# Kernel tuning notes

Hardware: AMD Instinct MI355X
Metric: run time of the kernel (lower is better)

Reference implementation:

```python
import jax, jax.numpy as jnp
import numpy as np

N = 100_000
E = 1_600_000
F_IN = 128
HEADS = 8
OUT_H = 8   # per-head channels, concat -> 64
N_CLS = 40
K_HOPS = 10  # truncation order of heat-kernel Taylor series
NEG_SLOPE = 0.2
T_INIT = 5.0


def setup_inputs() -> dict:
    key = jax.random.key(0)
    ks = jax.random.split(key, 10)
    x = jax.random.normal(ks[0], (N, F_IN), jnp.float32)
    edge_index = jax.random.randint(ks[1], (2, E), 0, N, jnp.int32)
    t = jnp.full((F_IN,), T_INIT, jnp.float32)  # per-channel learnable diffusion time
    W1 = jax.random.normal(ks[2], (F_IN, HEADS * OUT_H), jnp.float32) / np.sqrt(F_IN).astype(np.float32)
    a_src1 = jax.random.normal(ks[3], (HEADS, OUT_H), jnp.float32) * 0.1
    a_dst1 = jax.random.normal(ks[4], (HEADS, OUT_H), jnp.float32) * 0.1
    b1 = jnp.zeros((HEADS * OUT_H,), jnp.float32)
    W2 = jax.random.normal(ks[5], (HEADS * OUT_H, N_CLS), jnp.float32) / np.sqrt(HEADS * OUT_H).astype(np.float32)
    a_src2 = jax.random.normal(ks[6], (1, N_CLS), jnp.float32) * 0.1
    a_dst2 = jax.random.normal(ks[7], (1, N_CLS), jnp.float32) * 0.1
    b2 = jnp.zeros((N_CLS,), jnp.float32)
    return {"x": x, "edge_index": edge_index, "t": t, "W1": W1, "a_src1": a_src1,
            "a_dst1": a_dst1, "b1": b1, "W2": W2, "a_src2": a_src2, "a_dst2": a_dst2, "b2": b2}


def _add_self_loops(edge_index, n):
    loop = jnp.arange(n, dtype=edge_index.dtype)
    return jnp.concatenate([edge_index, jnp.stack([loop, loop])], axis=1)


def _diffusion(x, src, dst, t, n):
    # heat kernel: exp(-t) * sum_k t^k/k! * A_hat^k x, per-channel t
    deg = jax.ops.segment_sum(jnp.ones_like(src, jnp.float32), dst, num_segments=n)
    dinv = jnp.where(deg > 0, jax.lax.rsqrt(jnp.maximum(deg, 1.0)), 0.0)
    norm = dinv[src] * dinv[dst]  # [E+N]

    def prop(h):
        return jax.ops.segment_sum(norm[:, None] * h[src], dst, num_segments=n)

    coef0 = jnp.exp(-t)  # [F]

    def step(carry, k):
        h, coef, acc = carry
        h = prop(h)
        coef = coef * t / k
        return (h, coef, acc + coef * h), None

    (_, _, out), _ = jax.lax.scan(step, (x, coef0, coef0 * x),
                                  jnp.arange(1, K_HOPS + 1, dtype=jnp.float32))
    return out


def _gat_layer(x, src, dst, W, a_s, a_d, b, heads, out_ch, concat, n):
    h = (x @ W).reshape(n, heads, out_ch)                  # [N,H,C]
    al_s = jnp.einsum('nhc,hc->nh', h, a_s)                # src attn logits
    al_d = jnp.einsum('nhc,hc->nh', h, a_d)
    e = jax.nn.leaky_relu(al_s[src] + al_d[dst], NEG_SLOPE)  # [E+N, H]
    emax = jax.ops.segment_max(e, dst, num_segments=n)       # stable softmax per target node
    ex = jnp.exp(e - emax[dst])
    denom = jax.ops.segment_sum(ex, dst, num_segments=n)
    alpha = ex / jnp.maximum(denom[dst], 1e-16)               # [E+N, H]
    out = jax.ops.segment_sum(alpha[:, :, None] * h[src], dst, num_segments=n)  # [N,H,C]
    out = out.reshape(n, heads * out_ch) if concat else out.mean(axis=1)
    return out + b


def reference(x, edge_index, t, W1, a_src1, a_dst1, b1, W2, a_src2, a_dst2, b2):
    n = x.shape[0]
    ei = _add_self_loops(edge_index, n)
    src, dst = ei[0], ei[1]
    h = _diffusion(x, src, dst, t, n)
    h = _gat_layer(h, src, dst, W1, a_src1, a_dst1, b1, HEADS, OUT_H, True, n)
    h = jax.nn.elu(h)
    h = _gat_layer(h, src, dst, W2, a_src2, a_dst2, b2, 1, N_CLS, False, n)
    return jax.nn.log_softmax(h, axis=1)
```

## Files before the change

kernel.cpp:

```cpp
#include <hip/hip_runtime.h>
#include <hip/hip_bf16.h>


static __device__ __forceinline__ unsigned pack_bf16x2(float a, float b) {
    __hip_bfloat162 p(__float2bfloat16(a), __float2bfloat16(b));
    return *reinterpret_cast<unsigned*>(&p);
}

__global__ void init_node_kernel(int* deg, int* cursor, int n) {
    int i = blockIdx.x * 256 + threadIdx.x;
    if (i < n) { deg[i] = 1; cursor[i] = 0; }
}

__global__ void edge_deg_kernel(const int* __restrict__ dst, int* deg, int E) {
    int e = blockIdx.x * 256 + threadIdx.x;
    if (e < E) atomicAdd(&deg[dst[e]], 1);
}

__global__ void alloc_kernel(const int* __restrict__ deg, float* dinv,
                             int* row_off, int* gcount, int n) {
    int i = blockIdx.x * 256 + threadIdx.x;
    if (i >= n) return;
    int dg = deg[i];
    dinv[i] = rsqrtf((float)dg);
    row_off[i] = atomicAdd(gcount, dg);
}

__global__ void scatter_kernel(const int* __restrict__ ei, const int* __restrict__ row_off,
                               int* cursor, const float* __restrict__ dinv,
                               int2* csr_pair, int E, int n) {
    int e = blockIdx.x * 256 + threadIdx.x;
    if (e >= E + n) return;
    int s, d;
    if (e < E) { s = ei[e]; d = ei[E + e]; } else { s = e - E; d = s; }
    int pos = atomicAdd(&cursor[d], 1);
    int slot = row_off[d] + pos;
    csr_pair[slot] = make_int2(s, __float_as_int(dinv[s] * dinv[d]));
}

__global__ void coef_kernel(const float* __restrict__ t, float* coefs) {
    int c = threadIdx.x;
    float tc = t[c];
    float v = expf(-tc);
    coefs[c] = v;
    for (int k = 1; k <= 10; ++k) { v *= tc / (float)k; coefs[k * 128 + c] = v; }
}

__global__ void init_diff_kernel(const float4* __restrict__ x4, const float* __restrict__ coefs,
                                 uint2* __restrict__ h, float4* __restrict__ acc4, int total4) {
    int i = blockIdx.x * 256 + threadIdx.x;
    if (i >= total4) return;
    float4 xv = x4[i];
    h[i] = make_uint2(pack_bf16x2(xv.x, xv.y), pack_bf16x2(xv.z, xv.w));
    const float4 c = *(const float4*)&coefs[(i & 31) * 4];
    acc4[i] = make_float4(c.x * xv.x, c.y * xv.y, c.z * xv.z, c.w * xv.w);
}

__global__ void hop_kernel(const int* __restrict__ row_off, const int* __restrict__ deg,
                           const int2* __restrict__ csr_pair,
                           const unsigned* __restrict__ h, unsigned* __restrict__ h_next,
                           float2* __restrict__ acc2, const float2* __restrict__ coefk2,
                           int n, int write_h) {
    int wid = (blockIdx.x << 2) + (threadIdx.x >> 6);
    int lane = threadIdx.x & 63;
    if (wid >= n) return;
    int off = row_off[wid];
    int cnt = deg[wid];
    float2 a0 = {0.f, 0.f}, a1 = {0.f, 0.f}, a2 = {0.f, 0.f}, a3 = {0.f, 0.f};
    for (int base = 0; base < cnt; base += 64) {
        int nb = min(64, cnt - base);
        int2 p = {0, 0};
        if (lane < nb) p = csr_pair[off + base + lane];
        int tt = 0;
        for (; tt + 7 < nb; tt += 8) {
            int s0 = __builtin_amdgcn_readlane(p.x, tt);
            int s1 = __builtin_amdgcn_readlane(p.x, tt + 1);
            int s2 = __builtin_amdgcn_readlane(p.x, tt + 2);
            int s3 = __builtin_amdgcn_readlane(p.x, tt + 3);
            int s4 = __builtin_amdgcn_readlane(p.x, tt + 4);
            int s5 = __builtin_amdgcn_readlane(p.x, tt + 5);
            int s6 = __builtin_amdgcn_readlane(p.x, tt + 6);
            int s7 = __builtin_amdgcn_readlane(p.x, tt + 7);
            float w0 = __int_as_float(__builtin_amdgcn_readlane(p.y, tt));
            float w1 = __int_as_float(__builtin_amdgcn_readlane(p.y, tt + 1));
            float w2 = __int_as_float(__builtin_amdgcn_readlane(p.y, tt + 2));
            float w3 = __int_as_float(__builtin_amdgcn_readlane(p.y, tt + 3));
            float w4 = __int_as_float(__builtin_amdgcn_readlane(p.y, tt + 4));
            float w5 = __int_as_float(__builtin_amdgcn_readlane(p.y, tt + 5));
            float w6 = __int_as_float(__builtin_amdgcn_readlane(p.y, tt + 6));
            float w7 = __int_as_float(__builtin_amdgcn_readlane(p.y, tt + 7));
            unsigned u0 = h[(size_t)s0 * 64 + lane];
            unsigned u1 = h[(size_t)s1 * 64 + lane];
            unsigned u2 = h[(size_t)s2 * 64 + lane];
            unsigned u3 = h[(size_t)s3 * 64 + lane];
            unsigned u4 = h[(size_t)s4 * 64 + lane];
            unsigned u5 = h[(size_t)s5 * 64 + lane];
            unsigned u6 = h[(size_t)s6 * 64 + lane];
            unsigned u7 = h[(size_t)s7 * 64 + lane];
            a0.x = fmaf(w0, __uint_as_float(u0 << 16), a0.x);
            a0.y = fmaf(w0, __uint_as_float(u0 & 0xffff0000u), a0.y);
            a1.x = fmaf(w1, __uint_as_float(u1 << 16), a1.x);
            a1.y = fmaf(w1, __uint_as_float(u1 & 0xffff0000u), a1.y);
            a2.x = fmaf(w2, __uint_as_float(u2 << 16), a2.x);
            a2.y = fmaf(w2, __uint_as_float(u2 & 0xffff0000u), a2.y);
            a3.x = fmaf(w3, __uint_as_float(u3 << 16), a3.x);
            a3.y = fmaf(w3, __uint_as_float(u3 & 0xffff0000u), a3.y);
            a0.x = fmaf(w4, __uint_as_float(u4 << 16), a0.x);
            a0.y = fmaf(w4, __uint_as_float(u4 & 0xffff0000u), a0.y);
            a1.x = fmaf(w5, __uint_as_float(u5 << 16), a1.x);
            a1.y = fmaf(w5, __uint_as_float(u5 & 0xffff0000u), a1.y);
            a2.x = fmaf(w6, __uint_as_float(u6 << 16), a2.x);
            a2.y = fmaf(w6, __uint_as_float(u6 & 0xffff0000u), a2.y);
            a3.x = fmaf(w7, __uint_as_float(u7 << 16), a3.x);
            a3.y = fmaf(w7, __uint_as_float(u7 & 0xffff0000u), a3.y);
        }
        for (; tt < nb; ++tt) {
            int s = __builtin_amdgcn_readlane(p.x, tt);
            float w = __int_as_float(__builtin_amdgcn_readlane(p.y, tt));
            unsigned u = h[(size_t)s * 64 + lane];
            a0.x = fmaf(w, __uint_as_float(u << 16), a0.x);
            a0.y = fmaf(w, __uint_as_float(u & 0xffff0000u), a0.y);
        }
    }
    float2 s;
    s.x = (a0.x + a1.x) + (a2.x + a3.x);
    s.y = (a0.y + a1.y) + (a2.y + a3.y);
    size_t o = (size_t)wid * 64 + lane;
    if (write_h) h_next[o] = pack_bf16x2(s.x, s.y);
    float2 c = coefk2[lane];
    float2 av = acc2[o];
    av.x = fmaf(c.x, s.x, av.x);
    av.y = fmaf(c.y, s.y, av.y);
    acc2[o] = av;
}

__global__ __launch_bounds__(256) void gemm1_kernel(
    const float* __restrict__ acc, const float* __restrict__ W1,
    const float* __restrict__ a_s, const float* __restrict__ a_d,
    unsigned* __restrict__ h1b, float* __restrict__ als, float* __restrict__ ald, int n) {
    __shared__ float Wl[128 * 64];
    __shared__ float Al[4][16 * 128];
    for (int i = threadIdx.x; i < 128 * 64; i += 256) Wl[i] = W1[i];
    int w = threadIdx.x >> 6;
    int lane = threadIdx.x & 63;
    int node0 = (blockIdx.x * 4 + w) * 16;
    const float4* accv4 = (const float4*)acc;
    float4* Av4 = (float4*)Al[w];
#pragma unroll
    for (int i = 0; i < 8; ++i) {
        int f4 = i * 64 + lane;
        int g4 = node0 * 32 + f4;
        float4 v = (g4 < n * 32) ? accv4[g4] : make_float4(0.f, 0.f, 0.f, 0.f);
        Av4[f4] = v;
    }
    __syncthreads();
    float sums[16];
#pragma unroll
    for (int nd = 0; nd < 16; ++nd) sums[nd] = 0.f;
#pragma unroll 1
    for (int kc = 0; kc < 16; ++kc) {
        float wr[8];
#pragma unroll
        for (int i = 0; i < 8; ++i) wr[i] = Wl[(kc * 8 + i) * 64 + lane];
#pragma unroll
        for (int nd = 0; nd < 16; ++nd) {
            float4 a = *(const float4*)&Al[w][nd * 128 + kc * 8];
            float4 b = *(const float4*)&Al[w][nd * 128 + kc * 8 + 4];
            float s = sums[nd];
            s = fmaf(wr[0], a.x, s); s = fmaf(wr[1], a.y, s);
            s = fmaf(wr[2], a.z, s); s = fmaf(wr[3], a.w, s);
            s = fmaf(wr[4], b.x, s); s = fmaf(wr[5], b.y, s);
            s = fmaf(wr[6], b.z, s); s = fmaf(wr[7], b.w, s);
            sums[nd] = s;
        }
    }
    float asv = a_s[lane], adv = a_d[lane];
#pragma unroll
    for (int nd = 0; nd < 16; ++nd) {
        int node = node0 + nd;
        if (node >= n) break;
        float sum = sums[nd];
        float partner = __shfl_xor(sum, 1);
        if ((lane & 1) == 0) h1b[(size_t)node * 32 + (lane >> 1)] = pack_bf16x2(sum, partner);
        float vs = sum * asv;
        float vd = sum * adv;
        vs += __shfl_xor(vs, 1); vs += __shfl_xor(vs, 2); vs += __shfl_xor(vs, 4);
        vd += __shfl_xor(vd, 1); vd += __shfl_xor(vd, 2); vd += __shfl_xor(vd, 4);
        if ((lane & 7) == 0) {
            als[(size_t)node * 8 + (lane >> 3)] = vs;
            ald[(size_t)node * 8 + (lane >> 3)] = vd;
        }
    }
}

__global__ void agg1_kernel(const int* __restrict__ row_off, const int* __restrict__ deg,
                            const int2* __restrict__ csr_pair,
                            const unsigned* __restrict__ h1b, const float* __restrict__ als,
                            const float* __restrict__ ald, const float* __restrict__ b1,
                            float2* __restrict__ helu2, int n) {
    int wid = (blockIdx.x << 2) + (threadIdx.x >> 6);
    int lane = threadIdx.x & 63;
    if (wid >= n) return;
    int half = lane >> 5;
    int l = lane & 31;
    int head = l >> 2;
    int off = row_off[wid];
    int cnt = deg[wid];
    float aldv = ald[(size_t)wid * 8 + head];
    float dA = 0.f, dB = 0.f;
    float2 aA = {0.f, 0.f}, aB = {0.f, 0.f};
    for (int base = 0; base < cnt; base += 64) {
        int nb = min(64, cnt - base);
        int srcv = 0;
        if (lane < nb) srcv = csr_pair[off + base + lane].x;
        int j = 0;
        for (; j + 3 < nb; j += 4) {
            int sA0 = __builtin_amdgcn_readlane(srcv, j);
            int sA1 = __builtin_amdgcn_readlane(srcv, j + 1);
            int sB0 = __builtin_amdgcn_readlane(srcv, j + 2);
            int sB1 = __builtin_amdgcn_readlane(srcv, j + 3);
            int sA = half ? sA1 : sA0;
            int sB = half ? sB1 : sB0;
            float eA = als[(size_t)sA * 8 + head] + aldv;
            float eB = als[(size_t)sB * 8 + head] + aldv;
            eA = eA > 0.f ? eA : 0.2f * eA;
            eB = eB > 0.f ? eB : 0.2f * eB;
            float pA = __expf(eA);
            float pB = __expf(eB);
            unsigned uA = h1b[(size_t)sA * 32 + l];
            unsigned uB = h1b[(size_t)sB * 32 + l];
            dA += pA; dB += pB;
            aA.x = fmaf(pA, __uint_as_float(uA << 16), aA.x);
            aA.y = fmaf(pA, __uint_as_float(uA & 0xffff0000u), aA.y);
            aB.x = fmaf(pB, __uint_as_float(uB << 16), aB.x);
            aB.y = fmaf(pB, __uint_as_float(uB & 0xffff0000u), aB.y);
        }
        for (; j < nb; j += 2) {
            int s0 = __builtin_amdgcn_readlane(srcv, j);
            int s1 = (j + 1 < nb) ? __builtin_amdgcn_readlane(srcv, j + 1) : -1;
            int s = half ? s1 : s0;
            bool valid = s >= 0;
            int ss = valid ? s : 0;
            float e = als[(size_t)ss * 8 + head] + aldv;
            e = e > 0.f ? e : 0.2f * e;
            float p = valid ? __expf(e) : 0.f;
            unsigned u = h1b[(size_t)ss * 32 + l];
            dA += p;
            aA.x = fmaf(p, __uint_as_float(u << 16), aA.x);
            aA.y = fmaf(p, __uint_as_float(u & 0xffff0000u), aA.y);
        }
    }
    float d = dA + dB;
    float2 accv = make_float2(aA.x + aB.x, aA.y + aB.y);
    d += __shfl_xor(d, 32);
    accv.x += __shfl_xor(accv.x, 32);
    accv.y += __shfl_xor(accv.y, 32);
    if (half == 0) {
        float inv = 1.f / d;
        float ox = fmaf(accv.x, inv, b1[2 * l]);
        float oy = fmaf(accv.y, inv, b1[2 * l + 1]);
        ox = ox > 0.f ? ox : expm1f(ox);
        oy = oy > 0.f ? oy : expm1f(oy);
        helu2[(size_t)wid * 32 + l] = make_float2(ox, oy);
    }
}

__global__ __launch_bounds__(256) void gemm2_kernel(
    const float* __restrict__ helu, const float* __restrict__ W2,
    const float* __restrict__ a_s, const float* __restrict__ a_d,
    unsigned* __restrict__ h2b, float* __restrict__ als, float* __restrict__ ald, int n) {
    __shared__ float Wl[64 * 40];
    __shared__ float Al[4][16 * 64];
    for (int i = threadIdx.x; i < 64 * 40; i += 256) Wl[i] = W2[i];
    int w = threadIdx.x >> 6;
    int lane = threadIdx.x & 63;
    int node0 = (blockIdx.x * 4 + w) * 16;
    const float4* hv4 = (const float4*)helu;
    float4* Av4 = (float4*)Al[w];
#pragma unroll
    for (int i = 0; i < 4; ++i) {
        int f4 = i * 64 + lane;
        int g4 = node0 * 16 + f4;
        float4 v = (g4 < n * 16) ? hv4[g4] : make_float4(0.f, 0.f, 0.f, 0.f);
        Av4[f4] = v;
    }
    __syncthreads();
    bool act = lane < 40;
    int li = act ? lane : 0;
    float sums[16];
#pragma unroll
    for (int nd = 0; nd < 16; ++nd) sums[nd] = 0.f;
#pragma unroll 1
    for (int kc = 0; kc < 8; ++kc) {
        float wr[8];
#pragma unroll
        for (int i = 0; i < 8; ++i) wr[i] = Wl[(kc * 8 + i) * 40 + li];
#pragma unroll
        for (int nd = 0; nd < 16; ++nd) {
            float4 a = *(const float4*)&Al[w][nd * 64 + kc * 8];
            float4 b = *(const float4*)&Al[w][nd * 64 + kc * 8 + 4];
            float s = sums[nd];
            s = fmaf(wr[0], a.x, s); s = fmaf(wr[1], a.y, s);
            s = fmaf(wr[2], a.z, s); s = fmaf(wr[3], a.w, s);
            s = fmaf(wr[4], b.x, s); s = fmaf(wr[5], b.y, s);
            s = fmaf(wr[6], b.z, s); s = fmaf(wr[7], b.w, s);
            sums[nd] = s;
        }
    }
    float asv = act ? a_s[lane] : 0.f;
    float adv = act ? a_d[lane] : 0.f;
#pragma unroll
    for (int nd = 0; nd < 16; ++nd) {
        int node = node0 + nd;
        if (node >= n) break;
        float sum = sums[nd];
        float partner = __shfl_xor(sum, 1);
        if (act && (lane & 1) == 0) h2b[(size_t)node * 20 + (lane >> 1)] = pack_bf16x2(sum, partner);
        float vs = act ? sum * asv : 0.f;
        float vd = act ? sum * adv : 0.f;
#pragma unroll
        for (int i = 32; i >= 1; i >>= 1) { vs += __shfl_xor(vs, i); vd += __shfl_xor(vd, i); }
        if (lane == 0) { als[node] = vs; ald[node] = vd; }
    }
}

__global__ void agg2_kernel(const int* __restrict__ row_off, const int* __restrict__ deg,
                            const int2* __restrict__ csr_pair,
                            const unsigned* __restrict__ h2b, const float* __restrict__ als,
                            const float* __restrict__ ald, const float* __restrict__ b2,
                            float* __restrict__ out, int n) {
    int wid = (blockIdx.x << 2) + (threadIdx.x >> 6);
    int lane = threadIdx.x & 63;
    if (wid >= n) return;
    int half = lane >> 5;
    int l = lane & 31;
    bool act = l < 20;
    int li = act ? l : 0;
    int off = row_off[wid];
    int cnt = deg[wid];
    float aldv = ald[wid];
    float dA = 0.f, dB = 0.f;
    float2 aA = {0.f, 0.f}, aB = {0.f, 0.f};
    for (int base = 0; base < cnt; base += 64) {
        int nb = min(64, cnt - base);
        int srcv = 0;
        if (lane < nb) srcv = csr_pair[off + base + lane].x;
        int j = 0;
        for (; j + 3 < nb; j += 4) {
            int sA0 = __builtin_amdgcn_readlane(srcv, j);
            int sA1 = __builtin_amdgcn_readlane(srcv, j + 1);
            int sB0 = __builtin_amdgcn_readlane(srcv, j + 2);
            int sB1 = __builtin_amdgcn_readlane(srcv, j + 3);
            int sA = half ? sA1 : sA0;
            int sB = half ? sB1 : sB0;
            float eA = als[sA] + aldv;
            float eB = als[sB] + aldv;
            eA = eA > 0.f ? eA : 0.2f * eA;
            eB = eB > 0.f ? eB : 0.2f * eB;
            float pA = __expf(eA);
            float pB = __expf(eB);
            unsigned uA = h2b[(size_t)sA * 20 + li];
            unsigned uB = h2b[(size_t)sB * 20 + li];
            dA += pA; dB += pB;
            aA.x = fmaf(pA, __uint_as_float(uA << 16), aA.x);
            aA.y = fmaf(pA, __uint_as_float(uA & 0xffff0000u), aA.y);
            aB.x = fmaf(pB, __uint_as_float(uB << 16), aB.x);
            aB.y = fmaf(pB, __uint_as_float(uB & 0xffff0000u), aB.y);
        }
        for (; j < nb; j += 2) {
            int s0 = __builtin_amdgcn_readlane(srcv, j);
            int s1 = (j + 1 < nb) ? __builtin_amdgcn_readlane(srcv, j + 1) : -1;
            int s = half ? s1 : s0;
            bool valid = s >= 0;
            int ss = valid ? s : 0;
            float e = als[ss] + aldv;
            e = e > 0.f ? e : 0.2f * e;
            float p = valid ? __expf(e) : 0.f;
            unsigned u = h2b[(size_t)ss * 20 + li];
            dA += p;
            aA.x = fmaf(p, __uint_as_float(u << 16), aA.x);
            aA.y = fmaf(p, __uint_as_float(u & 0xffff0000u), aA.y);
        }
    }
    float d = dA + dB;
    float2 accv = make_float2(aA.x + aB.x, aA.y + aB.y);
    d += __shfl_xor(d, 32);
    accv.x += __shfl_xor(accv.x, 32);
    accv.y += __shfl_xor(accv.y, 32);
    float inv = 1.f / d;
    bool live = (half == 0) && act;
    float ox = live ? fmaf(accv.x, inv, b2[2 * l]) : -1e30f;
    float oy = live ? fmaf(accv.y, inv, b2[2 * l + 1]) : -1e30f;
    float vv = fmaxf(ox, oy);
#pragma unroll
    for (int i = 16; i >= 1; i >>= 1) vv = fmaxf(vv, __shfl_xor(vv, i));
    float ex = live ? (__expf(ox - vv) + __expf(oy - vv)) : 0.f;
#pragma unroll
    for (int i = 16; i >= 1; i >>= 1) ex += __shfl_xor(ex, i);
    if (live) {
        float lse = vv + logf(ex);
        *(float2*)&out[(size_t)wid * 40 + 2 * l] = make_float2(ox - lse, oy - lse);
    }
}

extern "C" void kernel_launch(void* const* d_in, const int* in_sizes, int n_in,
                              void* d_out, int out_size, void* d_ws, size_t ws_size,
                              hipStream_t stream) {
    const float* x    = (const float*)d_in[0];
    const int*   ei   = (const int*)d_in[1];
    const float* t    = (const float*)d_in[2];
    const float* W1   = (const float*)d_in[3];
    const float* a_s1 = (const float*)d_in[4];
    const float* a_d1 = (const float*)d_in[5];
    const float* b1   = (const float*)d_in[6];
    const float* W2   = (const float*)d_in[7];
    const float* a_s2 = (const float*)d_in[8];
    const float* a_d2 = (const float*)d_in[9];
    const float* b2   = (const float*)d_in[10];
    float* out = (float*)d_out;

    const int N = in_sizes[0] / 128;
    const int E = in_sizes[1] / 2;

    char* w = (char*)d_ws;
    auto carve = [&](size_t bytes) {
        void* p = (void*)w;
        w += (bytes + 255) & ~(size_t)255;
        return p;
    };
    int*      deg      = (int*)carve((size_t)N * 4);
    int*      cursor   = (int*)carve((size_t)N * 4);
    int*      row_off  = (int*)carve((size_t)N * 4);
    int*      gcount   = (int*)carve(256);
    float*    dinv     = (float*)carve((size_t)N * 4);
    int2*     csr_pair = (int2*)carve((size_t)(E + N) * 8);
    float*    coefs    = (float*)carve(11 * 128 * 4);
    float*    als1     = (float*)carve((size_t)N * 8 * 4);
    float*    ald1     = (float*)carve((size_t)N * 8 * 4);
    float*    als2     = (float*)carve((size_t)N * 4);
    float*    ald2     = (float*)carve((size_t)N * 4);
    unsigned* hA       = (unsigned*)carve((size_t)N * 64 * 4);
    unsigned* hB       = (unsigned*)carve((size_t)N * 64 * 4);
    float*    acc      = (float*)carve((size_t)N * 128 * 4);
    unsigned* h1b      = (unsigned*)carve((size_t)N * 32 * 4);
    float*    helu     = (float*)carve((size_t)N * 64 * 4);
    unsigned* h2b      = (unsigned*)carve((size_t)N * 20 * 4);

    dim3 blk(256);
    int gN = (N + 255) / 256;
    int gE = (E + 255) / 256;
    int gEN = (E + N + 255) / 256;
    int gW = (N + 3) / 4;
    int gT = (N + 63) / 64;

    init_node_kernel<<<gN, blk, 0, stream>>>(deg, cursor, N);
    hipMemsetAsync(gcount, 0, 4, stream);
    edge_deg_kernel<<<gE, blk, 0, stream>>>(ei + E, deg, E);
    alloc_kernel<<<gN, blk, 0, stream>>>(deg, dinv, row_off, gcount, N);
    scatter_kernel<<<gEN, blk, 0, stream>>>(ei, row_off, cursor, dinv, csr_pair, E, N);
    coef_kernel<<<1, 128, 0, stream>>>(t, coefs);
    init_diff_kernel<<<(N * 32 + 255) / 256, blk, 0, stream>>>(
        (const float4*)x, coefs, (uint2*)hA, (float4*)acc, N * 32);

    unsigned* hc = hA;
    unsigned* hn = hB;
    for (int k = 1; k <= 10; ++k) {
        hop_kernel<<<gW, blk, 0, stream>>>(row_off, deg, csr_pair, hc, hn, (float2*)acc,
                                           (const float2*)(coefs + k * 128), N,
                                           k < 10 ? 1 : 0);
        unsigned* tmp = hc; hc = hn; hn = tmp;
    }

    gemm1_kernel<<<gT, blk, 0, stream>>>(acc, W1, a_s1, a_d1, h1b, als1, ald1, N);
    agg1_kernel<<<gW, blk, 0, stream>>>(row_off, deg, csr_pair, h1b, als1, ald1, b1,
                                        (float2*)helu, N);
    gemm2_kernel<<<gT, blk, 0, stream>>>(helu, W2, a_s2, a_d2, h2b, als2, ald2, N);
    agg2_kernel<<<gW, blk, 0, stream>>>(row_off, deg, csr_pair, h2b, als2, ald2, b2, out, N);
}
```

Before: 1.311 ms.

## Fuse diffusion hops into one persistent cooperative kernel with register accumulators

Replaces the init kernel and ten per-hop launches with a single persistent cooperative kernel of 1536 blocks. Each wave owns up to 17 nodes and keeps their acc values in registers across hops, using grid.sync between hops, which removes the per-hop acc read-modify-write and the launch gaps. CSR construction also records each edge's slot from the degree atomic, so the separate cursor atomics in scatter go away. The cost is a hard node limit (NMAX*NWAVE must cover N), more register pressure with launch_bounds(256,6), grid-sync overhead, and a gather loop unrolled 4 instead of 8.

```diff
diff --git a/kernel.cpp b/kernel.cpp
--- a/kernel.cpp
+++ b/kernel.cpp
@@ -1,20 +1,27 @@
 #include <hip/hip_runtime.h>
 #include <hip/hip_bf16.h>
-
+#include <hip/hip_cooperative_groups.h>
+
+namespace cg = cooperative_groups;
+
+
+#define NBLK  1536
+#define NWAVE (NBLK * 4)
+#define NMAX  17
 
 static __device__ __forceinline__ unsigned pack_bf16x2(float a, float b) {
     __hip_bfloat162 p(__float2bfloat16(a), __float2bfloat16(b));
     return *reinterpret_cast<unsigned*>(&p);
 }
 
-__global__ void init_node_kernel(int* deg, int* cursor, int n) {
+__global__ void init_node_kernel(int* deg, int n) {
     int i = blockIdx.x * 256 + threadIdx.x;
-    if (i < n) { deg[i] = 1; cursor[i] = 0; }
-}
-
-__global__ void edge_deg_kernel(const int* __restrict__ dst, int* deg, int E) {
+    if (i < n) deg[i] = 1;
+}
+
+__global__ void edge_deg_kernel(const int* __restrict__ dst, int* deg, int* epos, int E) {
     int e = blockIdx.x * 256 + threadIdx.x;
-    if (e < E) atomicAdd(&deg[dst[e]], 1);
+    if (e < E) epos[e] = atomicAdd(&deg[dst[e]], 1);
 }
 
 __global__ void alloc_kernel(const int* __restrict__ deg, float* dinv,
@@ -27,15 +34,17 @@
 }
 
 __global__ void scatter_kernel(const int* __restrict__ ei, const int* __restrict__ row_off,
-                               int* cursor, const float* __restrict__ dinv,
-                               int2* csr_pair, int E, int n) {
+                               const int* __restrict__ epos, const float* __restrict__ dinv,
+                               int2* __restrict__ csr_pair, int E, int n) {
     int e = blockIdx.x * 256 + threadIdx.x;
-    if (e >= E + n) return;
-    int s, d;
-    if (e < E) { s = ei[e]; d = ei[E + e]; } else { s = e - E; d = s; }
-    int pos = atomicAdd(&cursor[d], 1);
-    int slot = row_off[d] + pos;
-    csr_pair[slot] = make_int2(s, __float_as_int(dinv[s] * dinv[d]));
+    if (e < E) {
+        int s = ei[e], d = ei[E + e];
+        csr_pair[row_off[d] + epos[e]] = make_int2(s, __float_as_int(dinv[s] * dinv[d]));
+    } else if (e < E + n) {
+        int i = e - E;
+        float di = dinv[i];
+        csr_pair[row_off[i]] = make_int2(i, __float_as_int(di * di));
+    }
 }
 
 __global__ void coef_kernel(const float* __restrict__ t, float* coefs) {
@@ -46,92 +55,96 @@
     for (int k = 1; k <= 10; ++k) { v *= tc / (float)k; coefs[k * 128 + c] = v; }
 }
 
-__global__ void init_diff_kernel(const float4* __restrict__ x4, const float* __restrict__ coefs,
-                                 uint2* __restrict__ h, float4* __restrict__ acc4, int total4) {
-    int i = blockIdx.x * 256 + threadIdx.x;
-    if (i >= total4) return;
-    float4 xv = x4[i];
-    h[i] = make_uint2(pack_bf16x2(xv.x, xv.y), pack_bf16x2(xv.z, xv.w));
-    const float4 c = *(const float4*)&coefs[(i & 31) * 4];
-    acc4[i] = make_float4(c.x * xv.x, c.y * xv.y, c.z * xv.z, c.w * xv.w);
-}
-
-__global__ void hop_kernel(const int* __restrict__ row_off, const int* __restrict__ deg,
-                           const int2* __restrict__ csr_pair,
-                           const unsigned* __restrict__ h, unsigned* __restrict__ h_next,
-                           float2* __restrict__ acc2, const float2* __restrict__ coefk2,
-                           int n, int write_h) {
+__global__ __launch_bounds__(256, 6) void diffuse_kernel(
+    const int* __restrict__ row_off, const int* __restrict__ deg,
+    const int2* __restrict__ csr_pair, const float2* __restrict__ x2,
+    const float* __restrict__ coefs, unsigned* __restrict__ hA,
+    unsigned* __restrict__ hB, float2* __restrict__ accg, int n) {
+    cg::grid_group grid = cg::this_grid();
     int wid = (blockIdx.x << 2) + (threadIdx.x >> 6);
     int lane = threadIdx.x & 63;
-    if (wid >= n) return;
-    int off = row_off[wid];
-    int cnt = deg[wid];
-    float2 a0 = {0.f, 0.f}, a1 = {0.f, 0.f}, a2 = {0.f, 0.f}, a3 = {0.f, 0.f};
-    for (int base = 0; base < cnt; base += 64) {
-        int nb = min(64, cnt - base);
-        int2 p = {0, 0};
-        if (lane < nb) p = csr_pair[off + base + lane];
-        int tt = 0;
-        for (; tt + 7 < nb; tt += 8) {
-            int s0 = __builtin_amdgcn_readlane(p.x, tt);
-            int s1 = __builtin_amdgcn_readlane(p.x, tt + 1);
-            int s2 = __builtin_amdgcn_readlane(p.x, tt + 2);
-            int s3 = __builtin_amdgcn_readlane(p.x, tt + 3);
-            int s4 = __builtin_amdgcn_readlane(p.x, tt + 4);
-            int s5 = __builtin_amdgcn_readlane(p.x, tt + 5);
-            int s6 = __builtin_amdgcn_readlane(p.x, tt + 6);
-            int s7 = __builtin_amdgcn_readlane(p.x, tt + 7);
-            float w0 = __int_as_float(__builtin_amdgcn_readlane(p.y, tt));
-            float w1 = __int_as_float(__builtin_amdgcn_readlane(p.y, tt + 1));
-            float w2 = __int_as_float(__builtin_amdgcn_readlane(p.y, tt + 2));
-            float w3 = __int_as_float(__builtin_amdgcn_readlane(p.y, tt + 3));
-            float w4 = __int_as_float(__builtin_amdgcn_readlane(p.y, tt + 4));
-            float w5 = __int_as_float(__builtin_amdgcn_readlane(p.y, tt + 5));
-            float w6 = __int_as_float(__builtin_amdgcn_readlane(p.y, tt + 6));
-            float w7 = __int_as_float(__builtin_amdgcn_readlane(p.y, tt + 7));
-            unsigned u0 = h[(size_t)s0 * 64 + lane];
-            unsigned u1 = h[(size_t)s1 * 64 + lane];
-            unsigned u2 = h[(size_t)s2 * 64 + lane];
-            unsigned u3 = h[(size_t)s3 * 64 + lane];
-            unsigned u4 = h[(size_t)s4 * 64 + lane];
-            unsigned u5 = h[(size_t)s5 * 64 + lane];
-            unsigned u6 = h[(size_t)s6 * 64 + lane];
-            unsigned u7 = h[(size_t)s7 * 64 + lane];
-            a0.x = fmaf(w0, __uint_as_float(u0 << 16), a0.x);
-            a0.y = fmaf(w0, __uint_as_float(u0 & 0xffff0000u), a0.y);
-            a1.x = fmaf(w1, __uint_as_float(u1 << 16), a1.x);
-            a1.y = fmaf(w1, __uint_as_float(u1 & 0xffff0000u), a1.y);
-            a2.x = fmaf(w2, __uint_as_float(u2 << 16), a2.x);
-            a2.y = fmaf(w2, __uint_as_float(u2 & 0xffff0000u), a2.y);
-            a3.x = fmaf(w3, __uint_as_float(u3 << 16), a3.x);
-            a3.y = fmaf(w3, __uint_as_float(u3 & 0xffff0000u), a3.y);
-            a0.x = fmaf(w4, __uint_as_float(u4 << 16), a0.x);
-            a0.y = fmaf(w4, __uint_as_float(u4 & 0xffff0000u), a0.y);
-            a1.x = fmaf(w5, __uint_as_float(u5 << 16), a1.x);
-            a1.y = fmaf(w5, __uint_as_float(u5 & 0xffff0000u), a1.y);
-            a2.x = fmaf(w6, __uint_as_float(u6 << 16), a2.x);
-            a2.y = fmaf(w6, __uint_as_float(u6 & 0xffff0000u), a2.y);
-            a3.x = fmaf(w7, __uint_as_float(u7 << 16), a3.x);
-            a3.y = fmaf(w7, __uint_as_float(u7 & 0xffff0000u), a3.y);
-        }
-        for (; tt < nb; ++tt) {
-            int s = __builtin_amdgcn_readlane(p.x, tt);
-            float w = __int_as_float(__builtin_amdgcn_readlane(p.y, tt));
-            unsigned u = h[(size_t)s * 64 + lane];
-            a0.x = fmaf(w, __uint_as_float(u << 16), a0.x);
-            a0.y = fmaf(w, __uint_as_float(u & 0xffff0000u), a0.y);
-        }
-    }
-    float2 s;
-    s.x = (a0.x + a1.x) + (a2.x + a3.x);
-    s.y = (a0.y + a1.y) + (a2.y + a3.y);
-    size_t o = (size_t)wid * 64 + lane;
-    if (write_h) h_next[o] = pack_bf16x2(s.x, s.y);
-    float2 c = coefk2[lane];
-    float2 av = acc2[o];
-    av.x = fmaf(c.x, s.x, av.x);
-    av.y = fmaf(c.y, s.y, av.y);
-    acc2[o] = av;
+    const float2* coefs2 = (const float2*)coefs;
+
+    float2 acc[NMAX];
+    float2 c0 = coefs2[lane];
+#pragma unroll
+    for (int j = 0; j < NMAX; ++j) {
+        int node = wid + j * NWAVE;
+        if (node < n) {
+            float2 xv = x2[(size_t)node * 64 + lane];
+            acc[j] = make_float2(c0.x * xv.x, c0.y * xv.y);
+            hA[(size_t)node * 64 + lane] = pack_bf16x2(xv.x, xv.y);
+        } else {
+            acc[j] = make_float2(0.f, 0.f);
+        }
+    }
+    grid.sync();
+
+    const unsigned* cur = hA;
+    unsigned* nxt = hB;
+#pragma unroll 1
+    for (int k = 1; k <= 10; ++k) {
+        float2 ck = coefs2[(size_t)k * 64 + lane];
+        bool wh = (k < 10);
+#pragma unroll
+        for (int j = 0; j < NMAX; ++j) {
+            int node = wid + j * NWAVE;
+            if (node < n) {
+                int off = row_off[node];
+                int cnt = deg[node];
+                float2 a0 = {0.f, 0.f}, a1 = {0.f, 0.f};
+                float2 a2 = {0.f, 0.f}, a3 = {0.f, 0.f};
+                for (int base = 0; base < cnt; base += 64) {
+                    int nb = min(64, cnt - base);
+                    int2 p = {0, 0};
+                    if (lane < nb) p = csr_pair[off + base + lane];
+                    int tt = 0;
+                    for (; tt + 3 < nb; tt += 4) {
+                        int s0 = __builtin_amdgcn_readlane(p.x, tt);
+                        int s1 = __builtin_amdgcn_readlane(p.x, tt + 1);
+                        int s2 = __builtin_amdgcn_readlane(p.x, tt + 2);
+                        int s3 = __builtin_amdgcn_readlane(p.x, tt + 3);
+                        float w0 = __int_as_float(__builtin_amdgcn_readlane(p.y, tt));
+                        float w1 = __int_as_float(__builtin_amdgcn_readlane(p.y, tt + 1));
+                        float w2 = __int_as_float(__builtin_amdgcn_readlane(p.y, tt + 2));
+                        float w3 = __int_as_float(__builtin_amdgcn_readlane(p.y, tt + 3));
+                        unsigned u0 = cur[(size_t)s0 * 64 + lane];
+                        unsigned u1 = cur[(size_t)s1 * 64 + lane];
+                        unsigned u2 = cur[(size_t)s2 * 64 + lane];
+                        unsigned u3 = cur[(size_t)s3 * 64 + lane];
+                        a0.x = fmaf(w0, __uint_as_float(u0 << 16), a0.x);
+                        a0.y = fmaf(w0, __uint_as_float(u0 & 0xffff0000u), a0.y);
+                        a1.x = fmaf(w1, __uint_as_float(u1 << 16), a1.x);
+                        a1.y = fmaf(w1, __uint_as_float(u1 & 0xffff0000u), a1.y);
+                        a2.x = fmaf(w2, __uint_as_float(u2 << 16), a2.x);
+                        a2.y = fmaf(w2, __uint_as_float(u2 & 0xffff0000u), a2.y);
+                        a3.x = fmaf(w3, __uint_as_float(u3 << 16), a3.x);
+                        a3.y = fmaf(w3, __uint_as_float(u3 & 0xffff0000u), a3.y);
+                    }
+                    for (; tt < nb; ++tt) {
+                        int s = __builtin_amdgcn_readlane(p.x, tt);
+                        float w = __int_as_float(__builtin_amdgcn_readlane(p.y, tt));
+                        unsigned u = cur[(size_t)s * 64 + lane];
+                        a0.x = fmaf(w, __uint_as_float(u << 16), a0.x);
+                        a0.y = fmaf(w, __uint_as_float(u & 0xffff0000u), a0.y);
+                    }
+                }
+                float2 s;
+                s.x = (a0.x + a1.x) + (a2.x + a3.x);
+                s.y = (a0.y + a1.y) + (a2.y + a3.y);
+                if (wh) nxt[(size_t)node * 64 + lane] = pack_bf16x2(s.x, s.y);
+                acc[j].x = fmaf(ck.x, s.x, acc[j].x);
+                acc[j].y = fmaf(ck.y, s.y, acc[j].y);
+            }
+        }
+        if (k < 10) grid.sync();
+        const unsigned* t = cur; cur = nxt; nxt = (unsigned*)t;
+    }
+#pragma unroll
+    for (int j = 0; j < NMAX; ++j) {
+        int node = wid + j * NWAVE;
+        if (node < n) accg[(size_t)node * 64 + lane] = acc[j];
+    }
 }
 
 __global__ __launch_bounds__(256) void gemm1_kernel(
@@ -429,10 +442,10 @@
         return p;
     };
     int*      deg      = (int*)carve((size_t)N * 4);
-    int*      cursor   = (int*)carve((size_t)N * 4);
     int*      row_off  = (int*)carve((size_t)N * 4);
     int*      gcount   = (int*)carve(256);
     float*    dinv     = (float*)carve((size_t)N * 4);
+    int*      epos     = (int*)carve((size_t)E * 4);
     int2*     csr_pair = (int2*)carve((size_t)(E + N) * 8);
     float*    coefs    = (float*)carve(11 * 128 * 4);
     float*    als1     = (float*)carve((size_t)N * 8 * 4);
@@ -453,22 +466,28 @@
     int gW = (N + 3) / 4;
     int gT = (N + 63) / 64;
 
-    init_node_kernel<<<gN, blk, 0, stream>>>(deg, cursor, N);
+    init_node_kernel<<<gN, blk, 0, stream>>>(deg, N);
     hipMemsetAsync(gcount, 0, 4, stream);
-    edge_deg_kernel<<<gE, blk, 0, stream>>>(ei + E, deg, E);
+    edge_deg_kernel<<<gE, blk, 0, stream>>>(ei + E, deg, epos, E);
     alloc_kernel<<<gN, blk, 0, stream>>>(deg, dinv, row_off, gcount, N);
-    scatter_kernel<<<gEN, blk, 0, stream>>>(ei, row_off, cursor, dinv, csr_pair, E, N);
+    scatter_kernel<<<gEN, blk, 0, stream>>>(ei, row_off, epos, dinv, csr_pair, E, N);
     coef_kernel<<<1, 128, 0, stream>>>(t, coefs);
-    init_diff_kernel<<<(N * 32 + 255) / 256, blk, 0, stream>>>(
-        (const float4*)x, coefs, (uint2*)hA, (float4*)acc, N * 32);
-
-    unsigned* hc = hA;
-    unsigned* hn = hB;
-    for (int k = 1; k <= 10; ++k) {
-        hop_kernel<<<gW, blk, 0, stream>>>(row_off, deg, csr_pair, hc, hn, (float2*)acc,
-                                           (const float2*)(coefs + k * 128), N,
-                                           k < 10 ? 1 : 0);
-        unsigned* tmp = hc; hc = hn; hn = tmp;
+
+    {
+        const float2* x2v = (const float2*)x;
+        float2* acc2v = (float2*)acc;
+        int Nv = N;
+        const int* row_off_v = row_off;
+        const int* deg_v = deg;
+        const int2* csr_v = csr_pair;
+        const float* coefs_v = coefs;
+        unsigned* hA_v = hA;
+        unsigned* hB_v = hB;
+        void* kargs[] = {(void*)&row_off_v, (void*)&deg_v, (void*)&csr_v, (void*)&x2v,
+                         (void*)&coefs_v, (void*)&hA_v, (void*)&hB_v, (void*)&acc2v,
+                         (void*)&Nv};
+        hipLaunchCooperativeKernel((const void*)diffuse_kernel, dim3(NBLK), dim3(256),
+                                   kargs, 0, stream);
     }
 
     gemm1_kernel<<<gT, blk, 0, stream>>>(acc, W1, a_s1, a_d1, h1b, als1, ald1, N);
```

Measured after the change: 3.305 ms. +152.1%, slower.

## Store all diffusion hops in bf16 and combine once; drop CSR cursor atomics

Applied to the files above, without the earlier changes.

When the workspace is large enough, each diffusion hop writes its bf16 output into its own buffer. A single combine kernel then forms the Taylor-weighted sum from x and all ten hops, so the fp32 accumulator is no longer read and written on every hop. CSR construction also reuses the slot index returned by the degree atomic, which removes the second atomic pass over a cursor array. In exchange the change needs roughly eleven bf16 feature buffers of workspace and an extra epos array. If the workspace is too small, it falls back to the old per-hop accumulation.

```diff
diff --git a/kernel.cpp b/kernel.cpp
--- a/kernel.cpp
+++ b/kernel.cpp
@@ -7,14 +7,14 @@
     return *reinterpret_cast<unsigned*>(&p);
 }
 
-__global__ void init_node_kernel(int* deg, int* cursor, int n) {
+__global__ void init_node_kernel(int* deg, int n) {
     int i = blockIdx.x * 256 + threadIdx.x;
-    if (i < n) { deg[i] = 1; cursor[i] = 0; }
-}
-
-__global__ void edge_deg_kernel(const int* __restrict__ dst, int* deg, int E) {
+    if (i < n) deg[i] = 1;
+}
+
+__global__ void edge_deg_kernel(const int* __restrict__ dst, int* deg, int* epos, int E) {
     int e = blockIdx.x * 256 + threadIdx.x;
-    if (e < E) atomicAdd(&deg[dst[e]], 1);
+    if (e < E) epos[e] = atomicAdd(&deg[dst[e]], 1);
 }
 
 __global__ void alloc_kernel(const int* __restrict__ deg, float* dinv,
@@ -27,15 +27,17 @@
 }
 
 __global__ void scatter_kernel(const int* __restrict__ ei, const int* __restrict__ row_off,
-                               int* cursor, const float* __restrict__ dinv,
-                               int2* csr_pair, int E, int n) {
+                               const int* __restrict__ epos, const float* __restrict__ dinv,
+                               int2* __restrict__ csr_pair, int E, int n) {
     int e = blockIdx.x * 256 + threadIdx.x;
-    if (e >= E + n) return;
-    int s, d;
-    if (e < E) { s = ei[e]; d = ei[E + e]; } else { s = e - E; d = s; }
-    int pos = atomicAdd(&cursor[d], 1);
-    int slot = row_off[d] + pos;
-    csr_pair[slot] = make_int2(s, __float_as_int(dinv[s] * dinv[d]));
+    if (e < E) {
+        int s = ei[e], d = ei[E + e];
+        csr_pair[row_off[d] + epos[e]] = make_int2(s, __float_as_int(dinv[s] * dinv[d]));
+    } else if (e < E + n) {
+        int i = e - E;
+        float di = dinv[i];
+        csr_pair[row_off[i]] = make_int2(i, __float_as_int(di * di));
+    }
 }
 
 __global__ void coef_kernel(const float* __restrict__ t, float* coefs) {
@@ -46,24 +48,28 @@
     for (int k = 1; k <= 10; ++k) { v *= tc / (float)k; coefs[k * 128 + c] = v; }
 }
 
-__global__ void init_diff_kernel(const float4* __restrict__ x4, const float* __restrict__ coefs,
-                                 uint2* __restrict__ h, float4* __restrict__ acc4, int total4) {
+__global__ void init_diff_a_kernel(const float4* __restrict__ x4, uint2* __restrict__ h0,
+                                   int total4) {
     int i = blockIdx.x * 256 + threadIdx.x;
     if (i >= total4) return;
     float4 xv = x4[i];
-    h[i] = make_uint2(pack_bf16x2(xv.x, xv.y), pack_bf16x2(xv.z, xv.w));
+    h0[i] = make_uint2(pack_bf16x2(xv.x, xv.y), pack_bf16x2(xv.z, xv.w));
+}
+
+__global__ void init_diff_b_kernel(const float4* __restrict__ x4, const float* __restrict__ coefs,
+                                   uint2* __restrict__ h0, float4* __restrict__ acc4, int total4) {
+    int i = blockIdx.x * 256 + threadIdx.x;
+    if (i >= total4) return;
+    float4 xv = x4[i];
+    h0[i] = make_uint2(pack_bf16x2(xv.x, xv.y), pack_bf16x2(xv.z, xv.w));
     const float4 c = *(const float4*)&coefs[(i & 31) * 4];
     acc4[i] = make_float4(c.x * xv.x, c.y * xv.y, c.z * xv.z, c.w * xv.w);
 }
 
-__global__ void hop_kernel(const int* __restrict__ row_off, const int* __restrict__ deg,
-                           const int2* __restrict__ csr_pair,
-                           const unsigned* __restrict__ h, unsigned* __restrict__ h_next,
-                           float2* __restrict__ acc2, const float2* __restrict__ coefk2,
-                           int n, int write_h) {
-    int wid = (blockIdx.x << 2) + (threadIdx.x >> 6);
-    int lane = threadIdx.x & 63;
-    if (wid >= n) return;
+static __device__ __forceinline__ float2 gather_row(
+    const int* __restrict__ row_off, const int* __restrict__ deg,
+    const int2* __restrict__ csr_pair, const unsigned* __restrict__ h,
+    int wid, int lane) {
     int off = row_off[wid];
     int cnt = deg[wid];
     float2 a0 = {0.f, 0.f}, a1 = {0.f, 0.f}, a2 = {0.f, 0.f}, a3 = {0.f, 0.f};
@@ -125,13 +131,56 @@
     float2 s;
     s.x = (a0.x + a1.x) + (a2.x + a3.x);
     s.y = (a0.y + a1.y) + (a2.y + a3.y);
+    return s;
+}
+
+__global__ void hop_a_kernel(const int* __restrict__ row_off, const int* __restrict__ deg,
+                             const int2* __restrict__ csr_pair,
+                             const unsigned* __restrict__ h_prev, unsigned* __restrict__ h_out,
+                             int n) {
+    int wid = (blockIdx.x << 2) + (threadIdx.x >> 6);
+    int lane = threadIdx.x & 63;
+    if (wid >= n) return;
+    float2 s = gather_row(row_off, deg, csr_pair, h_prev, wid, lane);
+    h_out[(size_t)wid * 64 + lane] = pack_bf16x2(s.x, s.y);
+}
+
+__global__ void hop_b_kernel(const int* __restrict__ row_off, const int* __restrict__ deg,
+                             const int2* __restrict__ csr_pair,
+                             const unsigned* __restrict__ h_prev, unsigned* __restrict__ h_out,
+                             float2* __restrict__ acc2, const float2* __restrict__ coefk2,
+                             int n, int write_h) {
+    int wid = (blockIdx.x << 2) + (threadIdx.x >> 6);
+    int lane = threadIdx.x & 63;
+    if (wid >= n) return;
+    float2 s = gather_row(row_off, deg, csr_pair, h_prev, wid, lane);
     size_t o = (size_t)wid * 64 + lane;
-    if (write_h) h_next[o] = pack_bf16x2(s.x, s.y);
+    if (write_h) h_out[o] = pack_bf16x2(s.x, s.y);
     float2 c = coefk2[lane];
     float2 av = acc2[o];
     av.x = fmaf(c.x, s.x, av.x);
     av.y = fmaf(c.y, s.y, av.y);
     acc2[o] = av;
+}
+
+__global__ void combine_kernel(const float2* __restrict__ x2, const float* __restrict__ coefs,
+                               const unsigned* __restrict__ hseq, size_t stride,
+                               float2* __restrict__ acc2, int total) {
+    int i = blockIdx.x * 256 + threadIdx.x;
+    if (i >= total) return;
+    int c2 = i & 63;
+    const float2* coefs2 = (const float2*)coefs;
+    float2 c0 = coefs2[c2];
+    float2 xv = x2[i];
+    float2 a = make_float2(c0.x * xv.x, c0.y * xv.y);
+#pragma unroll
+    for (int k = 1; k <= 10; ++k) {
+        float2 ck = coefs2[(size_t)k * 64 + c2];
+        unsigned u = hseq[(size_t)k * stride + i];
+        a.x = fmaf(ck.x, __uint_as_float(u << 16), a.x);
+        a.y = fmaf(ck.y, __uint_as_float(u & 0xffff0000u), a.y);
+    }
+    acc2[i] = a;
 }
 
 __global__ __launch_bounds__(256) void gemm1_kernel(
@@ -429,22 +478,27 @@
         return p;
     };
     int*      deg      = (int*)carve((size_t)N * 4);
-    int*      cursor   = (int*)carve((size_t)N * 4);
     int*      row_off  = (int*)carve((size_t)N * 4);
     int*      gcount   = (int*)carve(256);
     float*    dinv     = (float*)carve((size_t)N * 4);
+    int*      epos     = (int*)carve((size_t)E * 4);
     int2*     csr_pair = (int2*)carve((size_t)(E + N) * 8);
     float*    coefs    = (float*)carve(11 * 128 * 4);
     float*    als1     = (float*)carve((size_t)N * 8 * 4);
     float*    ald1     = (float*)carve((size_t)N * 8 * 4);
     float*    als2     = (float*)carve((size_t)N * 4);
     float*    ald2     = (float*)carve((size_t)N * 4);
-    unsigned* hA       = (unsigned*)carve((size_t)N * 64 * 4);
-    unsigned* hB       = (unsigned*)carve((size_t)N * 64 * 4);
     float*    acc      = (float*)carve((size_t)N * 128 * 4);
     unsigned* h1b      = (unsigned*)carve((size_t)N * 32 * 4);
     float*    helu     = (float*)carve((size_t)N * 64 * 4);
     unsigned* h2b      = (unsigned*)carve((size_t)N * 20 * 4);
+
+    size_t szh = (size_t)N * 64 * 4;
+    size_t used = (size_t)(w - (char*)d_ws);
+    size_t remain = (ws_size > used) ? ws_size - used : 0;
+    bool pathA = remain >= 11 * szh;
+    unsigned* hseq = (unsigned*)w;
+    size_t strideU = (size_t)N * 64;
 
     dim3 blk(256);
     int gN = (N + 255) / 256;
@@ -453,22 +507,36 @@
     int gW = (N + 3) / 4;
     int gT = (N + 63) / 64;
 
-    init_node_kernel<<<gN, blk, 0, stream>>>(deg, cursor, N);
+    init_node_kernel<<<gN, blk, 0, stream>>>(deg, N);
     hipMemsetAsync(gcount, 0, 4, stream);
-    edge_deg_kernel<<<gE, blk, 0, stream>>>(ei + E, deg, E);
+    edge_deg_kernel<<<gE, blk, 0, stream>>>(ei + E, deg, epos, E);
     alloc_kernel<<<gN, blk, 0, stream>>>(deg, dinv, row_off, gcount, N);
-    scatter_kernel<<<gEN, blk, 0, stream>>>(ei, row_off, cursor, dinv, csr_pair, E, N);
+    scatter_kernel<<<gEN, blk, 0, stream>>>(ei, row_off, epos, dinv, csr_pair, E, N);
     coef_kernel<<<1, 128, 0, stream>>>(t, coefs);
-    init_diff_kernel<<<(N * 32 + 255) / 256, blk, 0, stream>>>(
-        (const float4*)x, coefs, (uint2*)hA, (float4*)acc, N * 32);
-
-    unsigned* hc = hA;
-    unsigned* hn = hB;
-    for (int k = 1; k <= 10; ++k) {
-        hop_kernel<<<gW, blk, 0, stream>>>(row_off, deg, csr_pair, hc, hn, (float2*)acc,
-                                           (const float2*)(coefs + k * 128), N,
-                                           k < 10 ? 1 : 0);
-        unsigned* tmp = hc; hc = hn; hn = tmp;
+
+    if (pathA) {
+        init_diff_a_kernel<<<(N * 32 + 255) / 256, blk, 0, stream>>>(
+            (const float4*)x, (uint2*)hseq, N * 32);
+        for (int k = 1; k <= 10; ++k) {
+            hop_a_kernel<<<gW, blk, 0, stream>>>(row_off, deg, csr_pair,
+                                                 hseq + (size_t)(k - 1) * strideU,
+                                                 hseq + (size_t)k * strideU, N);
+        }
+        combine_kernel<<<(N * 64 + 255) / 256, blk, 0, stream>>>(
+            (const float2*)x, coefs, hseq, strideU, (float2*)acc, N * 64);
+    } else {
+        unsigned* hA = hseq;
+        unsigned* hB = hseq + strideU;
+        init_diff_b_kernel<<<(N * 32 + 255) / 256, blk, 0, stream>>>(
+            (const float4*)x, coefs, (uint2*)hA, (float4*)acc, N * 32);
+        unsigned* hc = hA;
+        unsigned* hn = hB;
+        for (int k = 1; k <= 10; ++k) {
+            hop_b_kernel<<<gW, blk, 0, stream>>>(row_off, deg, csr_pair, hc, hn, (float2*)acc,
+                                                 (const float2*)(coefs + k * 128), N,
+                                                 k < 10 ? 1 : 0);
+            unsigned* tmp = hc; hc = hn; hn = tmp;
+        }
     }
 
     gemm1_kernel<<<gT, blk, 0, stream>>>(acc, W1, a_s1, a_d1, h1b, als1, ald1, N);
```

Measured after the change: 1.274 ms. 2.8% less time.
